# Kernel tuning notes

Measured on AMD Instinct MI355X. Metric: run time of the kernel, lower is better.

## Reference

```python
import jax, jax.numpy as jnp
import numpy as np
from jax import lax

EPS = 1e-5

def _sign(x):
    # sign with sign(0)=+1, as used in XNOR-style binarization
    return jnp.where(x >= 0, 1.0, -1.0).astype(x.dtype)

def binarize(x):
    # straight-through estimator: forward = sign(x), backward = identity
    return x + lax.stop_gradient(_sign(x) - x)

def batchnorm(x, p):
    # p: [4, C] rows = (gamma, beta, running_mean, running_var); eval-mode BN
    g, b, m, v = p[0], p[1], p[2], p[3]
    shape = (1, -1) + (1,) * (x.ndim - 2)
    inv = g / jnp.sqrt(v + EPS)
    return (x - m.reshape(shape)) * inv.reshape(shape) + b.reshape(shape)

def conv2d(x, w):
    return lax.conv_general_dilated(x, w, window_strides=(1, 1), padding='VALID',
                                    dimension_numbers=('NCHW', 'OIHW', 'NCHW'))

def maxpool2(x):
    return lax.reduce_window(x, -jnp.inf, lax.max, (1, 1, 2, 2), (1, 1, 2, 2), 'VALID')

def hardtanh(x):
    return jnp.clip(x, -1.0, 1.0)


def setup_inputs() -> dict:
    key = jax.random.key(0)
    ks = jax.random.split(key, 16)
    B = 16384
    x = jax.random.normal(ks[0], (B, 3, 22, 22), jnp.float32)
    w1 = jax.random.normal(ks[1], (32, 3, 3, 3), jnp.float32) * 0.1
    w2 = jax.random.normal(ks[2], (32, 32, 3, 3), jnp.float32) * 0.1
    w3 = jax.random.normal(ks[3], (64, 32, 3, 3), jnp.float32) * 0.1
    w_fc1 = jax.random.normal(ks[4], (128, 64), jnp.float32) * 0.1
    w_fc2 = jax.random.normal(ks[5], (2, 128), jnp.float32) * 0.1
    w_fc3 = jax.random.normal(ks[6], (4, 128), jnp.float32) * 0.1

    def make_bn(k, c):
        k1, k2, k3, k4 = jax.random.split(k, 4)
        gamma = jax.random.uniform(k1, (c,), jnp.float32, 0.5, 1.5)
        beta = jax.random.normal(k2, (c,), jnp.float32) * 0.1
        mean = jax.random.normal(k3, (c,), jnp.float32) * 0.1
        var = jax.random.uniform(k4, (c,), jnp.float32, 0.5, 1.5)
        return jnp.stack([gamma, beta, mean, var])  # [4, C]

    bn1 = make_bn(ks[7], 32)
    bn2 = make_bn(ks[8], 32)
    bn3 = make_bn(ks[9], 64)
    bn4 = make_bn(ks[10], 128)
    bn5 = make_bn(ks[11], 2)
    bn6 = make_bn(ks[12], 4)
    return {'x': x, 'w1': w1, 'w2': w2, 'w3': w3, 'w_fc1': w_fc1, 'w_fc2': w_fc2,
            'w_fc3': w_fc3, 'bn1': bn1, 'bn2': bn2, 'bn3': bn3, 'bn4': bn4,
            'bn5': bn5, 'bn6': bn6}


def reference(x, w1, w2, w3, w_fc1, w_fc2, w_fc3, bn1, bn2, bn3, bn4, bn5, bn6):
    # binary=True, binarize_input=True, bitwidth=input_bitwidth=1:
    # every BinarizeConv2d/BinarizeLinear binarizes both its input and weights.
    h = hardtanh(batchnorm(conv2d(binarize(x), binarize(w1)), bn1))   # [B,32,20,20]
    h = maxpool2(h)                                                    # [B,32,10,10]
    h = hardtanh(batchnorm(conv2d(binarize(h), binarize(w2)), bn2))   # [B,32,8,8]
    h = maxpool2(h)                                                    # [B,32,4,4]
    h = hardtanh(batchnorm(conv2d(binarize(h), binarize(w3)), bn3))   # [B,64,2,2]
    h = maxpool2(h)                                                    # [B,64,1,1]
    h = h.reshape(-1, 64)                                              # [B,64]
    h = hardtanh(batchnorm(binarize(h) @ binarize(w_fc1).T, bn4))      # [B,128]
    out1 = jax.nn.softmax(batchnorm(h @ w_fc2.T, bn5), axis=1)         # [B,2]
    out2 = batchnorm(h @ w_fc3.T, bn6)                                 # [B,4]
    return (out1, out2)
```

## Files before the change

kernel.cpp:

```cpp
#include <hip/hip_runtime.h>
#include <cstdint>
#include <cmath>

#define OFF_W1   0
#define OFF_T1   32
#define OFF_W2   64
#define OFF_T2   352
#define OFF_W3   384
#define OFF_T3   960
#define OFF_WFC1 1024
#define OFF_A4   1280
#define OFF_C4   1408
#define OFF_WF2  1536
#define OFF_WF3  1792
#define OFF_BN5  2304
#define OFF_BN6  2308

__device__ __forceinline__ int thr_neg(double nterms, double g, double b, double m, double v) {
    double inv = g / sqrt(v + 1e-5);
    double t = m - b / inv;
    double thr = floor((nterms - t) * 0.5);
    if (thr < -2147000000.0) thr = -2147000000.0;
    if (thr >  2147000000.0) thr =  2147000000.0;
    return -((int)thr + 1);
}

__global__ void k_prep(const float* __restrict__ w1, const float* __restrict__ w2,
                       const float* __restrict__ w3, const float* __restrict__ wfc1,
                       const float* __restrict__ wfc2, const float* __restrict__ wfc3,
                       const float* __restrict__ bn1, const float* __restrict__ bn2,
                       const float* __restrict__ bn3, const float* __restrict__ bn4,
                       const float* __restrict__ bn5, const float* __restrict__ bn6,
                       unsigned int* __restrict__ ws) {
    __shared__ float stage[9216];
    int t = threadIdx.x;
    int blk = blockIdx.x;
    float* wsf = (float*)ws;
    int*   wsi = (int*)ws;

    if (blk == 0) {
        for (int i = t; i < 864; i += 256) stage[i] = w1[i];
        __syncthreads();
        if (t < 32) {
            unsigned int bits = 0;
            for (int j = 0; j < 27; ++j) bits |= (stage[t*27+j] >= 0.f ? 1u : 0u) << j;
            ws[OFF_W1 + t] = bits;
            wsi[OFF_T1 + t] = thr_neg(27.0,  bn1[t], bn1[32+t], bn1[64+t], bn1[96+t]);
            wsi[OFF_T2 + t] = thr_neg(288.0, bn2[t], bn2[32+t], bn2[64+t], bn2[96+t]);
        }
        for (int i = t; i < 256; i += 256) wsf[OFF_WF2 + i] = wfc2[i];
        for (int i = t; i < 512; i += 256) wsf[OFF_WF3 + i] = wfc3[i];
        if (t < 2) {
            float g = bn5[t], b = bn5[2+t], m = bn5[4+t], v = bn5[6+t];
            float inv = g / sqrtf(v + 1e-5f);
            wsf[OFF_BN5 + t]     = inv;
            wsf[OFF_BN5 + 2 + t] = b - m * inv;
        }
        if (t >= 4 && t < 8) {
            int j = t - 4;
            float g = bn6[j], b = bn6[4+j], m = bn6[8+j], v = bn6[12+j];
            float inv = g / sqrtf(v + 1e-5f);
            wsf[OFF_BN6 + j]     = inv;
            wsf[OFF_BN6 + 4 + j] = b - m * inv;
        }
    } else if (blk == 1) {
        for (int i = t; i < 9216; i += 256) stage[i] = w2[i];
        __syncthreads();
        for (int idx = t; idx < 288; idx += 256) {
            int o = idx / 9, k = idx - o*9;
            unsigned int bits = 0;
            for (int i = 0; i < 32; ++i)
                bits |= (stage[(o*32+i)*9 + k] >= 0.f ? 1u : 0u) << i;
            ws[OFF_W2 + idx] = bits;
        }
    } else if (blk == 2 || blk == 3) {
        int base = (blk - 2) * 9216;
        for (int i = t; i < 9216; i += 256) stage[i] = w3[base + i];
        __syncthreads();
        for (int idx = t; idx < 288; idx += 256) {
            int o = idx / 9, k = idx - o*9;
            unsigned int bits = 0;
            for (int i = 0; i < 32; ++i)
                bits |= (stage[(o*32+i)*9 + k] >= 0.f ? 1u : 0u) << i;
            ws[OFF_W3 + base/32 + idx] = bits;
        }
    } else {
        for (int i = t; i < 8192; i += 256) stage[i] = wfc1[i];
        __syncthreads();
        if (t < 128) {
            unsigned int lo = 0, hi = 0;
            for (int j = 0; j < 32; ++j) lo |= (stage[t*64+j]    >= 0.f ? 1u : 0u) << j;
            for (int j = 0; j < 32; ++j) hi |= (stage[t*64+32+j] >= 0.f ? 1u : 0u) << j;
            ws[OFF_WFC1 + 2*t]     = lo;
            ws[OFF_WFC1 + 2*t + 1] = hi;
            float g = bn4[t], b = bn4[128+t], m = bn4[256+t], v = bn4[384+t];
            float inv = g / sqrtf(v + 1e-5f);
            wsf[OFF_A4 + t] = -2.f * inv;
            wsf[OFF_C4 + t] = (64.f - m) * inv + b;
        }
        if (t >= 128 && t < 192) {
            int j = t - 128;
            wsi[OFF_T3 + j] = thr_neg(288.0, bn3[j], bn3[64+j], bn3[128+j], bn3[192+j]);
        }
    }
}

#define WSTRIDE 584
__global__ __launch_bounds__(256) void k_main(const float* __restrict__ x,
                                              const unsigned int* __restrict__ ws,
                                              float* __restrict__ out, int B) {
    __shared__ unsigned int s_u[4 * WSTRIDE];

    const int tid = threadIdx.x & 63;
    const int wid = threadIdx.x >> 6;
    const int b   = blockIdx.x * 4 + wid;
    if (b >= B) return;
    const float* wsf = (const float*)ws;
    const int*   wsi = (const int*)ws;

    unsigned int* inrow = s_u + wid * WSTRIDE;
    unsigned int* c1    = inrow + 66;
    unsigned int* pb1   = c1 + 400;
    unsigned int* pb2   = pb1 + 100;

    for (int r = tid; r < 66; r += 64) {
        int c = r / 22, y = r - c*22;
        const float2* p = (const float2*)(x + ((size_t)b*3 + c)*484 + (size_t)y*22);
        unsigned int bits = 0;
        #pragma unroll
        for (int j = 0; j < 11; ++j) {
            float2 v = p[j];
            bits |= (v.x >= 0.f ? 1u : 0u) << (2*j);
            bits |= (v.y >= 0.f ? 1u : 0u) << (2*j+1);
        }
        inrow[r] = bits;
    }
    __builtin_amdgcn_wave_barrier();

    for (int pos = tid; pos < 400; pos += 64) {
        int y = pos / 20, xx = pos - y*20;
        unsigned int g = 0;
        #pragma unroll
        for (int c = 0; c < 3; ++c)
            #pragma unroll
            for (int dy = 0; dy < 3; ++dy)
                g |= ((inrow[c*22 + y + dy] >> xx) & 7u) << (c*9 + dy*3);
        unsigned int word = 0;
        #pragma unroll
        for (int o = 31; o >= 0; --o) {
            unsigned int s = (unsigned int)(__popc(g ^ ws[OFF_W1 + o]) + wsi[OFF_T1 + o]);
            word = __builtin_amdgcn_alignbit(word, s, 31);
        }
        c1[pos] = word;
    }
    __builtin_amdgcn_wave_barrier();

    for (int p = tid; p < 100; p += 64) {
        int py = p / 10, px = p - py*10;
        int base = (2*py)*20 + 2*px;
        pb1[p] = c1[base] | c1[base+1] | c1[base+20] | c1[base+21];
    }
    __builtin_amdgcn_wave_barrier();

    {
        int y = tid >> 3, xx = tid & 7;
        unsigned int in9[9];
        #pragma unroll
        for (int dy = 0; dy < 3; ++dy)
            #pragma unroll
            for (int dx = 0; dx < 3; ++dx)
                in9[dy*3+dx] = pb1[(y+dy)*10 + xx + dx];
        unsigned int word = 0;
        #pragma unroll
        for (int o = 31; o >= 0; --o) {
            int s = wsi[OFF_T2 + o];
            #pragma unroll
            for (int k = 0; k < 9; ++k)
                s += __popc(in9[k] ^ ws[OFF_W2 + o*9 + k]);
            word = __builtin_amdgcn_alignbit(word, (unsigned int)s, 31);
        }
        word |= __shfl_xor(word, 1);
        word |= __shfl_xor(word, 8);
        if ((tid & 9) == 0)
            pb2[(y>>1)*4 + (xx>>1)] = word;
    }
    __builtin_amdgcn_wave_barrier();

    unsigned long long b3 = 0;
    {
        unsigned int bb[16];
        #pragma unroll
        for (int i = 0; i < 16; ++i) bb[i] = pb2[i];
        unsigned int w3r[9];
        #pragma unroll
        for (int k = 0; k < 9; ++k) w3r[k] = ws[OFF_W3 + tid*9 + k];
        int negt = wsi[OFF_T3 + tid];
        unsigned int oracc = 0;
        #pragma unroll
        for (int py = 0; py < 2; ++py)
            #pragma unroll
            for (int px = 0; px < 2; ++px) {
                int s = negt;
                #pragma unroll
                for (int dy = 0; dy < 3; ++dy)
                    #pragma unroll
                    for (int dx = 0; dx < 3; ++dx)
                        s += __popc(bb[(py+dy)*4 + px + dx] ^ w3r[dy*3+dx]);
                oracc |= (unsigned int)s;
            }
        b3 = __ballot((int)oracc < 0);
    }

    float h0, h1;
    {
        const unsigned long long* wfc1b = (const unsigned long long*)(ws + OFF_WFC1);
        int pc0 = __popcll(b3 ^ wfc1b[tid]);
        int pc1 = __popcll(b3 ^ wfc1b[tid + 64]);
        float p0 = fmaf((float)pc0, wsf[OFF_A4 + tid],      wsf[OFF_C4 + tid]);
        float p1 = fmaf((float)pc1, wsf[OFF_A4 + tid + 64], wsf[OFF_C4 + tid + 64]);
        h0 = fminf(1.f, fmaxf(-1.f, p0));
        h1 = fminf(1.f, fmaxf(-1.f, p1));
    }

    {
        float part[6];
        #pragma unroll
        for (int j = 0; j < 2; ++j)
            part[j] = h0 * wsf[OFF_WF2 + j*128 + tid] + h1 * wsf[OFF_WF2 + j*128 + 64 + tid];
        #pragma unroll
        for (int j = 0; j < 4; ++j)
            part[2+j] = h0 * wsf[OFF_WF3 + j*128 + tid] + h1 * wsf[OFF_WF3 + j*128 + 64 + tid];
        #pragma unroll
        for (int off = 32; off; off >>= 1) {
            #pragma unroll
            for (int j = 0; j < 6; ++j)
                part[j] += __shfl_xor(part[j], off);
        }
        if (tid < 6) {
            if (tid < 2) {
                float y0 = part[0]*wsf[OFF_BN5+0] + wsf[OFF_BN5+2];
                float y1 = part[1]*wsf[OFF_BN5+1] + wsf[OFF_BN5+3];
                float mx = fmaxf(y0, y1);
                float e0 = expf(y0 - mx), e1 = expf(y1 - mx);
                float r  = 1.f / (e0 + e1);
                out[(size_t)b*2 + tid] = (tid == 0 ? e0 : e1) * r;
            } else {
                int j = tid - 2;
                out[(size_t)B*2 + (size_t)b*4 + j] = part[2+j]*wsf[OFF_BN6+j] + wsf[OFF_BN6+4+j];
            }
        }
    }
}

extern "C" void kernel_launch(void* const* d_in, const int* in_sizes, int n_in,
                              void* d_out, int out_size, void* d_ws, size_t ws_size,
                              hipStream_t stream) {
    const float* x    = (const float*)d_in[0];
    const float* w1   = (const float*)d_in[1];
    const float* w2   = (const float*)d_in[2];
    const float* w3   = (const float*)d_in[3];
    const float* wfc1 = (const float*)d_in[4];
    const float* wfc2 = (const float*)d_in[5];
    const float* wfc3 = (const float*)d_in[6];
    const float* bn1  = (const float*)d_in[7];
    const float* bn2  = (const float*)d_in[8];
    const float* bn3  = (const float*)d_in[9];
    const float* bn4  = (const float*)d_in[10];
    const float* bn5  = (const float*)d_in[11];
    const float* bn6  = (const float*)d_in[12];
    unsigned int* ws  = (unsigned int*)d_ws;
    float* out        = (float*)d_out;
    int B = in_sizes[0] / 1452;

    k_prep<<<5, 256, 0, stream>>>(w1, w2, w3, wfc1, wfc2, wfc3,
                                  bn1, bn2, bn3, bn4, bn5, bn6, ws);
    k_main<<<(B + 3) / 4, 256, 0, stream>>>(x, ws, out, B);
}
```

Measured before the change: 190.0 us.

## Process two images per wavefront to amortize weight loads and overheads

Each wavefront now handles two batch images instead of one, so every weight and threshold load from the workspace is reused across both images in all conv and FC stages. Input sign-binarization switches from float compares to alignbit on the raw sign bits followed by an inversion, and launch bounds now request 8 blocks per CU. The cost is double the shared memory per block and higher register pressure, which may lower occupancy, while the reduction shuffles double.

```diff
diff --git a/kernel.cpp b/kernel.cpp
--- a/kernel.cpp
+++ b/kernel.cpp
@@ -106,134 +106,177 @@
 }
 
 #define WSTRIDE 584
-__global__ __launch_bounds__(256) void k_main(const float* __restrict__ x,
-                                              const unsigned int* __restrict__ ws,
-                                              float* __restrict__ out, int B) {
-    __shared__ unsigned int s_u[4 * WSTRIDE];
+#define AB(a,b) __builtin_amdgcn_alignbit(a, b, 31)
+__global__ __launch_bounds__(256, 8) void k_main(const float* __restrict__ x,
+                                                 const unsigned int* __restrict__ ws,
+                                                 float* __restrict__ out, int B) {
+    __shared__ unsigned int s_u[8 * WSTRIDE];
 
     const int tid = threadIdx.x & 63;
     const int wid = threadIdx.x >> 6;
-    const int b   = blockIdx.x * 4 + wid;
-    if (b >= B) return;
+    const int b0  = blockIdx.x * 8 + wid * 2;
+    if (b0 >= B) return;
+    const bool act1 = (b0 + 1 < B);
+    const int  b1   = act1 ? b0 + 1 : b0;
     const float* wsf = (const float*)ws;
     const int*   wsi = (const int*)ws;
 
-    unsigned int* inrow = s_u + wid * WSTRIDE;
-    unsigned int* c1    = inrow + 66;
-    unsigned int* pb1   = c1 + 400;
-    unsigned int* pb2   = pb1 + 100;
+    unsigned int* in0 = s_u + (wid*2) * WSTRIDE;
+    unsigned int* in1 = in0 + WSTRIDE;
+    unsigned int* c10 = in0 + 66;
+    unsigned int* c11 = in1 + 66;
+    unsigned int* pA0 = c10 + 400;
+    unsigned int* pA1 = c11 + 400;
+    unsigned int* pB0 = pA0 + 100;
+    unsigned int* pB1 = pA1 + 100;
 
     for (int r = tid; r < 66; r += 64) {
         int c = r / 22, y = r - c*22;
-        const float2* p = (const float2*)(x + ((size_t)b*3 + c)*484 + (size_t)y*22);
-        unsigned int bits = 0;
-        #pragma unroll
-        for (int j = 0; j < 11; ++j) {
-            float2 v = p[j];
-            bits |= (v.x >= 0.f ? 1u : 0u) << (2*j);
-            bits |= (v.y >= 0.f ? 1u : 0u) << (2*j+1);
-        }
-        inrow[r] = bits;
+        const uint2* p0 = (const uint2*)(x + ((size_t)b0*3 + c)*484 + (size_t)y*22);
+        const uint2* p1 = (const uint2*)(x + ((size_t)b1*3 + c)*484 + (size_t)y*22);
+        uint2 q0[11], q1[11];
+        #pragma unroll
+        for (int j = 0; j < 11; ++j) { q0[j] = p0[j]; q1[j] = p1[j]; }
+        unsigned int s0 = 0, s1 = 0;
+        #pragma unroll
+        for (int j = 10; j >= 0; --j) {
+            s0 = AB(s0, q0[j].y); s0 = AB(s0, q0[j].x);
+            s1 = AB(s1, q1[j].y); s1 = AB(s1, q1[j].x);
+        }
+        in0[r] = ~s0;
+        in1[r] = ~s1;
     }
     __builtin_amdgcn_wave_barrier();
 
     for (int pos = tid; pos < 400; pos += 64) {
         int y = pos / 20, xx = pos - y*20;
-        unsigned int g = 0;
+        unsigned int g0 = 0, g1 = 0;
         #pragma unroll
         for (int c = 0; c < 3; ++c)
             #pragma unroll
-            for (int dy = 0; dy < 3; ++dy)
-                g |= ((inrow[c*22 + y + dy] >> xx) & 7u) << (c*9 + dy*3);
-        unsigned int word = 0;
+            for (int dy = 0; dy < 3; ++dy) {
+                g0 |= ((in0[c*22 + y + dy] >> xx) & 7u) << (c*9 + dy*3);
+                g1 |= ((in1[c*22 + y + dy] >> xx) & 7u) << (c*9 + dy*3);
+            }
+        unsigned int w0 = 0, w1 = 0;
         #pragma unroll
         for (int o = 31; o >= 0; --o) {
-            unsigned int s = (unsigned int)(__popc(g ^ ws[OFF_W1 + o]) + wsi[OFF_T1 + o]);
-            word = __builtin_amdgcn_alignbit(word, s, 31);
-        }
-        c1[pos] = word;
+            unsigned int wv = ws[OFF_W1 + o];
+            int tv = wsi[OFF_T1 + o];
+            unsigned int s0 = (unsigned int)(__popc(g0 ^ wv) + tv);
+            unsigned int s1 = (unsigned int)(__popc(g1 ^ wv) + tv);
+            w0 = AB(w0, s0);
+            w1 = AB(w1, s1);
+        }
+        c10[pos] = w0;
+        c11[pos] = w1;
     }
     __builtin_amdgcn_wave_barrier();
 
     for (int p = tid; p < 100; p += 64) {
         int py = p / 10, px = p - py*10;
         int base = (2*py)*20 + 2*px;
-        pb1[p] = c1[base] | c1[base+1] | c1[base+20] | c1[base+21];
+        pA0[p] = c10[base] | c10[base+1] | c10[base+20] | c10[base+21];
+        pA1[p] = c11[base] | c11[base+1] | c11[base+20] | c11[base+21];
     }
     __builtin_amdgcn_wave_barrier();
 
     {
         int y = tid >> 3, xx = tid & 7;
-        unsigned int in9[9];
+        unsigned int a9[9], b9[9];
         #pragma unroll
         for (int dy = 0; dy < 3; ++dy)
             #pragma unroll
-            for (int dx = 0; dx < 3; ++dx)
-                in9[dy*3+dx] = pb1[(y+dy)*10 + xx + dx];
-        unsigned int word = 0;
+            for (int dx = 0; dx < 3; ++dx) {
+                a9[dy*3+dx] = pA0[(y+dy)*10 + xx + dx];
+                b9[dy*3+dx] = pA1[(y+dy)*10 + xx + dx];
+            }
+        unsigned int w0 = 0, w1 = 0;
         #pragma unroll
         for (int o = 31; o >= 0; --o) {
-            int s = wsi[OFF_T2 + o];
-            #pragma unroll
-            for (int k = 0; k < 9; ++k)
-                s += __popc(in9[k] ^ ws[OFF_W2 + o*9 + k]);
-            word = __builtin_amdgcn_alignbit(word, (unsigned int)s, 31);
-        }
-        word |= __shfl_xor(word, 1);
-        word |= __shfl_xor(word, 8);
-        if ((tid & 9) == 0)
-            pb2[(y>>1)*4 + (xx>>1)] = word;
+            int t2 = wsi[OFF_T2 + o];
+            int s0 = t2, s1 = t2;
+            #pragma unroll
+            for (int k = 0; k < 9; ++k) {
+                unsigned int wv = ws[OFF_W2 + o*9 + k];
+                s0 += __popc(a9[k] ^ wv);
+                s1 += __popc(b9[k] ^ wv);
+            }
+            w0 = AB(w0, (unsigned int)s0);
+            w1 = AB(w1, (unsigned int)s1);
+        }
+        w0 |= __shfl_xor(w0, 1);  w1 |= __shfl_xor(w1, 1);
+        w0 |= __shfl_xor(w0, 8);  w1 |= __shfl_xor(w1, 8);
+        if ((tid & 9) == 0) {
+            pB0[(y>>1)*4 + (xx>>1)] = w0;
+            pB1[(y>>1)*4 + (xx>>1)] = w1;
+        }
     }
     __builtin_amdgcn_wave_barrier();
 
-    unsigned long long b3 = 0;
+    unsigned long long b3[2];
     {
-        unsigned int bb[16];
-        #pragma unroll
-        for (int i = 0; i < 16; ++i) bb[i] = pb2[i];
         unsigned int w3r[9];
         #pragma unroll
         for (int k = 0; k < 9; ++k) w3r[k] = ws[OFF_W3 + tid*9 + k];
         int negt = wsi[OFF_T3 + tid];
-        unsigned int oracc = 0;
-        #pragma unroll
-        for (int py = 0; py < 2; ++py)
-            #pragma unroll
-            for (int px = 0; px < 2; ++px) {
-                int s = negt;
+        #pragma unroll
+        for (int im = 0; im < 2; ++im) {
+            const unsigned int* pb = im ? pB1 : pB0;
+            unsigned int bb[16];
+            #pragma unroll
+            for (int i = 0; i < 16; ++i) bb[i] = pb[i];
+            unsigned int oracc = 0;
+            #pragma unroll
+            for (int py = 0; py < 2; ++py)
                 #pragma unroll
-                for (int dy = 0; dy < 3; ++dy)
+                for (int px = 0; px < 2; ++px) {
+                    int s = negt;
                     #pragma unroll
-                    for (int dx = 0; dx < 3; ++dx)
-                        s += __popc(bb[(py+dy)*4 + px + dx] ^ w3r[dy*3+dx]);
-                oracc |= (unsigned int)s;
-            }
-        b3 = __ballot((int)oracc < 0);
-    }
-
-    float h0, h1;
+                    for (int dy = 0; dy < 3; ++dy)
+                        #pragma unroll
+                        for (int dx = 0; dx < 3; ++dx)
+                            s += __popc(bb[(py+dy)*4 + px + dx] ^ w3r[dy*3+dx]);
+                    oracc |= (unsigned int)s;
+                }
+            b3[im] = __ballot((int)oracc < 0);
+        }
+    }
+
+    float h0a, h1a, h0b, h1b;
     {
         const unsigned long long* wfc1b = (const unsigned long long*)(ws + OFF_WFC1);
-        int pc0 = __popcll(b3 ^ wfc1b[tid]);
-        int pc1 = __popcll(b3 ^ wfc1b[tid + 64]);
-        float p0 = fmaf((float)pc0, wsf[OFF_A4 + tid],      wsf[OFF_C4 + tid]);
-        float p1 = fmaf((float)pc1, wsf[OFF_A4 + tid + 64], wsf[OFF_C4 + tid + 64]);
-        h0 = fminf(1.f, fmaxf(-1.f, p0));
-        h1 = fminf(1.f, fmaxf(-1.f, p1));
+        unsigned long long wlo = wfc1b[tid], whi = wfc1b[tid + 64];
+        float a4l = wsf[OFF_A4 + tid], c4l = wsf[OFF_C4 + tid];
+        float a4h = wsf[OFF_A4 + tid + 64], c4h = wsf[OFF_C4 + tid + 64];
+        float p0 = fmaf((float)__popcll(b3[0] ^ wlo), a4l, c4l);
+        float p1 = fmaf((float)__popcll(b3[0] ^ whi), a4h, c4h);
+        float p2 = fmaf((float)__popcll(b3[1] ^ wlo), a4l, c4l);
+        float p3 = fmaf((float)__popcll(b3[1] ^ whi), a4h, c4h);
+        h0a = fminf(1.f, fmaxf(-1.f, p0));
+        h1a = fminf(1.f, fmaxf(-1.f, p1));
+        h0b = fminf(1.f, fmaxf(-1.f, p2));
+        h1b = fminf(1.f, fmaxf(-1.f, p3));
     }
 
     {
-        float part[6];
-        #pragma unroll
-        for (int j = 0; j < 2; ++j)
-            part[j] = h0 * wsf[OFF_WF2 + j*128 + tid] + h1 * wsf[OFF_WF2 + j*128 + 64 + tid];
-        #pragma unroll
-        for (int j = 0; j < 4; ++j)
-            part[2+j] = h0 * wsf[OFF_WF3 + j*128 + tid] + h1 * wsf[OFF_WF3 + j*128 + 64 + tid];
+        float part[12];
+        #pragma unroll
+        for (int j = 0; j < 2; ++j) {
+            float wl = wsf[OFF_WF2 + j*128 + tid], wh = wsf[OFF_WF2 + j*128 + 64 + tid];
+            part[j]     = h0a * wl + h1a * wh;
+            part[6 + j] = h0b * wl + h1b * wh;
+        }
+        #pragma unroll
+        for (int j = 0; j < 4; ++j) {
+            float wl = wsf[OFF_WF3 + j*128 + tid], wh = wsf[OFF_WF3 + j*128 + 64 + tid];
+            part[2 + j]  = h0a * wl + h1a * wh;
+            part[8 + j]  = h0b * wl + h1b * wh;
+        }
         #pragma unroll
         for (int off = 32; off; off >>= 1) {
             #pragma unroll
-            for (int j = 0; j < 6; ++j)
+            for (int j = 0; j < 12; ++j)
                 part[j] += __shfl_xor(part[j], off);
         }
         if (tid < 6) {
@@ -243,10 +286,20 @@
                 float mx = fmaxf(y0, y1);
                 float e0 = expf(y0 - mx), e1 = expf(y1 - mx);
                 float r  = 1.f / (e0 + e1);
-                out[(size_t)b*2 + tid] = (tid == 0 ? e0 : e1) * r;
+                out[(size_t)b0*2 + tid] = (tid == 0 ? e0 : e1) * r;
+                if (act1) {
+                    float z0 = part[6]*wsf[OFF_BN5+0] + wsf[OFF_BN5+2];
+                    float z1 = part[7]*wsf[OFF_BN5+1] + wsf[OFF_BN5+3];
+                    float mz = fmaxf(z0, z1);
+                    float f0 = expf(z0 - mz), f1 = expf(z1 - mz);
+                    float rz = 1.f / (f0 + f1);
+                    out[(size_t)b1*2 + tid] = (tid == 0 ? f0 : f1) * rz;
+                }
             } else {
                 int j = tid - 2;
-                out[(size_t)B*2 + (size_t)b*4 + j] = part[2+j]*wsf[OFF_BN6+j] + wsf[OFF_BN6+4+j];
+                out[(size_t)B*2 + (size_t)b0*4 + j] = part[2+j]*wsf[OFF_BN6+j] + wsf[OFF_BN6+4+j];
+                if (act1)
+                    out[(size_t)B*2 + (size_t)b1*4 + j] = part[8+j]*wsf[OFF_BN6+j] + wsf[OFF_BN6+4+j];
             }
         }
     }
@@ -274,5 +327,5 @@
 
     k_prep<<<5, 256, 0, stream>>>(w1, w2, w3, wfc1, wfc2, wfc3,
                                   bn1, bn2, bn3, bn4, bn5, bn6, ws);
-    k_main<<<(B + 3) / 4, 256, 0, stream>>>(x, ws, out, B);
+    k_main<<<(B + 7) / 8, 256, 0, stream>>>(x, ws, out, B);
 }
```

New measurement: 197.3 us. 1.04x slower.

## Coalesce input binarization via ballot, optionally split into separate extract kernel

Applied to the files above, without the earlier changes.

The input load changes from per-row strided float2 reads to fully coalesced per-wave contiguous loads, with the sign bits packed by __ballot into a 46-word bitstream. Rows are then recovered with alignbit. If workspace is large enough, a separate k_extract kernel writes the packed bits to workspace first, and k_main reads only those. k_main also gains a launch_bounds occupancy hint. The extra kernel launch and bitmap round-trip cost some overhead, in exchange for better memory coalescing on the dominant input read.

```diff
diff --git a/kernel.cpp b/kernel.cpp
--- a/kernel.cpp
+++ b/kernel.cpp
@@ -15,6 +15,7 @@
 #define OFF_WF3  1792
 #define OFF_BN5  2304
 #define OFF_BN6  2308
+#define OFF_BM   4096
 
 __device__ __forceinline__ int thr_neg(double nterms, double g, double b, double m, double v) {
     double inv = g / sqrt(v + 1e-5);
@@ -105,10 +106,45 @@
     }
 }
 
+__global__ __launch_bounds__(256) void k_extract(const float* __restrict__ x,
+                                                 unsigned int* __restrict__ bm,
+                                                 int B) {
+    const int tid = threadIdx.x & 63;
+    const int wid = threadIdx.x >> 6;
+    const int b   = blockIdx.x * 4 + wid;
+    if (b >= B) return;
+    const unsigned int base = (unsigned int)b * 1452u;
+    const unsigned int last = (unsigned int)B * 1452u - 1u;
+    unsigned int keep = 0;
+    #pragma unroll 1
+    for (int c = 0; c < 3; ++c) {
+        const int kb = c * 8, kn = (c == 2) ? 7 : 8;
+        float v[8];
+        #pragma unroll
+        for (int k = 0; k < 8; ++k)
+            if (k < kn) {
+                unsigned int idx = base + (unsigned int)(kb + k) * 64u + (unsigned int)tid;
+                if (idx > last) idx = last;
+                v[k] = x[idx];
+            }
+        #pragma unroll
+        for (int k = 0; k < 8; ++k)
+            if (k < kn) {
+                unsigned long long m = __ballot(v[k] >= 0.f);
+                int w2k = (kb + k) * 2;
+                if (tid == w2k)     keep = (unsigned int)m;
+                if (tid == w2k + 1) keep = (unsigned int)(m >> 32);
+            }
+    }
+    if (tid < 46) bm[(size_t)b * 46 + tid] = keep;
+}
+
 #define WSTRIDE 584
-__global__ __launch_bounds__(256) void k_main(const float* __restrict__ x,
-                                              const unsigned int* __restrict__ ws,
-                                              float* __restrict__ out, int B) {
+#define AB31(a,b) __builtin_amdgcn_alignbit(a, b, 31)
+__global__ __launch_bounds__(256, 8) void k_main(const float* __restrict__ x,
+                                                 const unsigned int* __restrict__ ws,
+                                                 float* __restrict__ out, int B,
+                                                 int use_bm) {
     __shared__ unsigned int s_u[4 * WSTRIDE];
 
     const int tid = threadIdx.x & 63;
@@ -118,22 +154,42 @@
     const float* wsf = (const float*)ws;
     const int*   wsi = (const int*)ws;
 
-    unsigned int* inrow = s_u + wid * WSTRIDE;
-    unsigned int* c1    = inrow + 66;
-    unsigned int* pb1   = c1 + 400;
-    unsigned int* pb2   = pb1 + 100;
+    unsigned int* in   = s_u + wid * WSTRIDE;
+    unsigned int* c1   = in + 66;
+    unsigned int* pb1  = c1 + 400;
+    unsigned int* pb2  = pb1 + 100;
+
+    if (use_bm) {
+        if (tid < 46) c1[tid] = ws[OFF_BM + (size_t)b * 46 + tid];
+    } else {
+        unsigned long long* bal = (unsigned long long*)c1;
+        const unsigned int base = (unsigned int)b * 1452u;
+        const unsigned int last = (unsigned int)B * 1452u - 1u;
+        #pragma unroll 1
+        for (int c = 0; c < 3; ++c) {
+            const int kb = c * 8, kn = (c == 2) ? 7 : 8;
+            float v[8];
+            #pragma unroll
+            for (int k = 0; k < 8; ++k)
+                if (k < kn) {
+                    unsigned int idx = base + (unsigned int)(kb + k) * 64u + (unsigned int)tid;
+                    if (idx > last) idx = last;
+                    v[k] = x[idx];
+                }
+            #pragma unroll
+            for (int k = 0; k < 8; ++k)
+                if (k < kn) {
+                    unsigned long long m = __ballot(v[k] >= 0.f);
+                    if (tid == 0) bal[kb + k] = m;
+                }
+        }
+    }
+    __builtin_amdgcn_wave_barrier();
 
     for (int r = tid; r < 66; r += 64) {
-        int c = r / 22, y = r - c*22;
-        const float2* p = (const float2*)(x + ((size_t)b*3 + c)*484 + (size_t)y*22);
-        unsigned int bits = 0;
-        #pragma unroll
-        for (int j = 0; j < 11; ++j) {
-            float2 v = p[j];
-            bits |= (v.x >= 0.f ? 1u : 0u) << (2*j);
-            bits |= (v.y >= 0.f ? 1u : 0u) << (2*j+1);
-        }
-        inrow[r] = bits;
+        int bitpos = r * 22;
+        int wi = bitpos >> 5, sh = bitpos & 31;
+        in[r] = __builtin_amdgcn_alignbit(c1[wi + 1], c1[wi], sh);
     }
     __builtin_amdgcn_wave_barrier();
 
@@ -144,12 +200,12 @@
         for (int c = 0; c < 3; ++c)
             #pragma unroll
             for (int dy = 0; dy < 3; ++dy)
-                g |= ((inrow[c*22 + y + dy] >> xx) & 7u) << (c*9 + dy*3);
+                g |= ((in[c*22 + y + dy] >> xx) & 7u) << (c*9 + dy*3);
         unsigned int word = 0;
         #pragma unroll
         for (int o = 31; o >= 0; --o) {
             unsigned int s = (unsigned int)(__popc(g ^ ws[OFF_W1 + o]) + wsi[OFF_T1 + o]);
-            word = __builtin_amdgcn_alignbit(word, s, 31);
+            word = AB31(word, s);
         }
         c1[pos] = word;
     }
@@ -177,7 +233,7 @@
             #pragma unroll
             for (int k = 0; k < 9; ++k)
                 s += __popc(in9[k] ^ ws[OFF_W2 + o*9 + k]);
-            word = __builtin_amdgcn_alignbit(word, (unsigned int)s, 31);
+            word = AB31(word, (unsigned int)s);
         }
         word |= __shfl_xor(word, 1);
         word |= __shfl_xor(word, 8);
@@ -272,7 +328,12 @@
     float* out        = (float*)d_out;
     int B = in_sizes[0] / 1452;
 
+    size_t need = (size_t)OFF_BM * 4 + (size_t)B * 46 * 4;
+    int use_bm = (ws_size >= need) ? 1 : 0;
+
+    if (use_bm)
+        k_extract<<<(B + 3) / 4, 256, 0, stream>>>(x, ws + OFF_BM, B);
     k_prep<<<5, 256, 0, stream>>>(w1, w2, w3, wfc1, wfc2, wfc3,
                                   bn1, bn2, bn3, bn4, bn5, bn6, ws);
-    k_main<<<(B + 3) / 4, 256, 0, stream>>>(x, ws, out, B);
-}
+    k_main<<<(B + 3) / 4, 256, 0, stream>>>(x, ws, out, B, use_bm);
+}
```

Result: slower. 216.1 us (+13.8%).
